# Optimization experiments

Hardware: AMD Instinct MI355X
Metric: run time of the kernel (lower is better)

## Reference

```python
import jax, jax.numpy as jnp
import numpy as np

COMPRESSION = 2  # max-pool factor along flattened spatial axis for phi and g


def setup_inputs() -> dict:
    key = jax.random.key(0)
    ks = jax.random.split(key, 5)
    B, C, H, W = 4, 64, 96, 96
    Ci = 32  # intermediate_dim = C // 2
    s = 1.0 / np.sqrt(C)
    return {
        "x": jax.random.normal(ks[0], (B, C, H, W), dtype=jnp.float32),
        "w_theta": jax.random.normal(ks[1], (Ci, C), dtype=jnp.float32) * s,
        "b_theta": jnp.zeros((Ci,), dtype=jnp.float32),
        "w_phi": jax.random.normal(ks[2], (Ci, C), dtype=jnp.float32) * s,
        "b_phi": jnp.zeros((Ci,), dtype=jnp.float32),
        "w_g": jax.random.normal(ks[3], (Ci, C), dtype=jnp.float32) * s,
        "b_g": jnp.zeros((Ci,), dtype=jnp.float32),
        "w_out": jax.random.normal(ks[4], (C, Ci), dtype=jnp.float32) * (1.0 / np.sqrt(Ci)),
        "b_out": jnp.zeros((C,), dtype=jnp.float32),
    }


def reference(x, w_theta, b_theta, w_phi, b_phi, w_g, b_g, w_out, b_out):
    B, C, H, W = x.shape
    N = H * W
    xf = x.reshape(B, C, N).transpose(0, 2, 1)            # [B, N, C]
    # 1x1 conv projections == channel matmuls
    theta = xf @ w_theta.T + b_theta                      # [B, N, Ci]
    phi = xf @ w_phi.T + b_phi                            # [B, N, Ci]
    g = xf @ w_g.T + b_g                                  # [B, N, Ci]
    # compression: max-pool (kernel=stride=COMPRESSION) along flattened spatial axis
    Ci = theta.shape[-1]
    phi = phi.reshape(B, N // COMPRESSION, COMPRESSION, Ci).max(axis=2)  # [B, N/c, Ci]
    g = g.reshape(B, N // COMPRESSION, COMPRESSION, Ci).max(axis=2)      # [B, N/c, Ci]
    # embedded-gaussian affinity + softmax
    attn = jax.nn.softmax(jnp.einsum('bnc,bmc->bnm', theta, phi), axis=-1)  # [B, N, N/c]
    y = jnp.einsum('bnm,bmc->bnc', attn, g)               # [B, N, Ci]
    out = y @ w_out.T + b_out                             # [B, N, C]
    out = out.transpose(0, 2, 1).reshape(B, C, H, W)
    return out + x  # residual
```

## Files before the change

### kernel.cpp

```cpp
#include <hip/hip_runtime.h>
#include <hip/hip_bf16.h>


#define NQ 9216
#define MM 4608
#define TPW 36
#define LOG2E 1.44269504088896340736f

typedef __attribute__((ext_vector_type(8))) short bf16x8;
typedef __attribute__((ext_vector_type(4))) float f32x4;
typedef __attribute__((ext_vector_type(4))) unsigned short u16x4;

static __device__ __forceinline__ unsigned pk2(float a, float b) {
    __hip_bfloat162 h = __float22bfloat162_rn(make_float2(a, b));
    return *reinterpret_cast<unsigned*>(&h);
}

__global__ __launch_bounds__(128, 4) void proj_kernel(
    const float* __restrict__ x,
    const float* __restrict__ wt, const float* __restrict__ bt,
    const float* __restrict__ wp, const float* __restrict__ bp,
    const float* __restrict__ wg, const float* __restrict__ bg,
    unsigned short* __restrict__ theta, unsigned short* __restrict__ phi,
    unsigned short* __restrict__ gT)
{
    __shared__ unsigned short gst[32 * 20];

    const int tid  = threadIdx.x;
    const int wid  = tid >> 6;
    const int lane = tid & 63;
    const int q = lane >> 4;
    const int c = lane & 15;

    const int b     = blockIdx.x / 288;
    const int rem   = blockIdx.x % 288;
    const int n0    = rem * 32 + wid * 16;

    const float* Wm[3] = {wt, wp, wg};
    const float* Bm[3] = {bt, bp, bg};

    bf16x8 wf[3][2][2];
    float bias[3][2];
#pragma unroll
    for (int p = 0; p < 3; ++p) {
#pragma unroll
        for (int ct = 0; ct < 2; ++ct) {
            bias[p][ct] = Bm[p][ct * 16 + c];
#pragma unroll
            for (int ks = 0; ks < 2; ++ks) {
                const float* wsrc = Wm[p] + (ct * 16 + c) * 64 + ks * 32 + q * 8;
                f32x4 w0 = *(const f32x4*)wsrc;
                f32x4 w1 = *(const f32x4*)(wsrc + 4);
                unsigned* wk = (unsigned*)&wf[p][ct][ks];
                wk[0] = pk2(w0[0], w0[1]); wk[1] = pk2(w0[2], w0[3]);
                wk[2] = pk2(w1[0], w1[1]); wk[3] = pk2(w1[2], w1[3]);
            }
        }
    }

    bf16x8 af[2];
#pragma unroll
    for (int ks = 0; ks < 2; ++ks) {
        unsigned* ap = (unsigned*)&af[ks];
#pragma unroll
        for (int j2 = 0; j2 < 4; ++j2) {
            float x0 = x[(b * 64 + ks * 32 + q * 8 + j2 * 2) * NQ + n0 + c];
            float x1 = x[(b * 64 + ks * 32 + q * 8 + j2 * 2 + 1) * NQ + n0 + c];
            ap[j2] = pk2(x0, x1);
        }
    }

#pragma unroll
    for (int p = 0; p < 3; ++p) {
#pragma unroll
        for (int ct = 0; ct < 2; ++ct) {
            f32x4 acc = {0.f, 0.f, 0.f, 0.f};
            acc = __builtin_amdgcn_mfma_f32_16x16x32_bf16(af[0], wf[p][ct][0], acc, 0, 0, 0);
            acc = __builtin_amdgcn_mfma_f32_16x16x32_bf16(af[1], wf[p][ct][1], acc, 0, 0, 0);
#pragma unroll
            for (int r = 0; r < 4; ++r) acc[r] += bias[p][ct];
            const int ci = ct * 16 + c;
            if (p == 0) {
                unsigned pv0 = pk2(acc[0] * LOG2E, acc[1] * LOG2E);
                unsigned pv1 = pk2(acc[2] * LOG2E, acc[3] * LOG2E);
                theta[(b * NQ + n0 + 4 * q + 0) * 32 + ci] = (unsigned short)pv0;
                theta[(b * NQ + n0 + 4 * q + 1) * 32 + ci] = (unsigned short)(pv0 >> 16);
                theta[(b * NQ + n0 + 4 * q + 2) * 32 + ci] = (unsigned short)pv1;
                theta[(b * NQ + n0 + 4 * q + 3) * 32 + ci] = (unsigned short)(pv1 >> 16);
            } else {
                unsigned pv = pk2(fmaxf(acc[0], acc[1]), fmaxf(acc[2], acc[3]));
                if (p == 1) {
                    const int m0 = (n0 >> 1) + 2 * q;
                    phi[(b * MM + m0) * 32 + ci]     = (unsigned short)pv;
                    phi[(b * MM + m0 + 1) * 32 + ci] = (unsigned short)(pv >> 16);
                } else {
                    *(unsigned int*)(gst + ci * 20 + wid * 8 + 2 * q) = pv;
                }
            }
        }
    }

    __syncthreads();
    {
        const int ci = tid >> 2;
        const int m4 = (tid & 3) * 4;
        u16x4 v = *(const u16x4*)(gst + ci * 20 + m4);
        *(u16x4*)(gT + (b * 32 + ci) * MM + rem * 16 + m4) = v;
    }
}

__global__ __launch_bounds__(256, 4) void attn_kernel(
    const unsigned short* __restrict__ theta, const unsigned short* __restrict__ phi,
    const unsigned short* __restrict__ gT,
    unsigned short* __restrict__ y)
{
    __shared__ unsigned short pld[4][48 * 32];
    __shared__ float red[4][48][36];
    __shared__ float lred[4][48];

    const int tid  = threadIdx.x;
    const int w    = tid >> 6;
    const int lane = tid & 63;
    const int q  = lane >> 4;
    const int c  = lane & 15;
    const int sw = ((c >> 1) & 3) << 3;

    const int b  = blockIdx.x / 192;
    const int nb = (blockIdx.x % 192) * 48;

    bf16x8 qf[3];
#pragma unroll
    for (int rt = 0; rt < 3; ++rt)
        qf[rt] = *(const bf16x8*)(theta + (b * NQ + nb + rt * 16 + c) * 32 + q * 8);

    const unsigned short* phiB = phi + (size_t)b * MM * 32;
    const unsigned short* gTB  = gT + (size_t)b * 32 * MM;
    unsigned short* myp = pld[w];

    f32x4 acc[3][2];
    float lsum[3];
#pragma unroll
    for (int rt = 0; rt < 3; ++rt) {
        lsum[rt] = 0.f;
#pragma unroll
        for (int s2 = 0; s2 < 2; ++s2) acc[rt][s2] = (f32x4){0.f, 0.f, 0.f, 0.f};
    }

    const int t0 = w * TPW;
    bf16x8 kf[2], vf[2];

#define LOAD_KF(m0) do {                                                      \
    kf[0] = *(const bf16x8*)(phiB + ((m0) + c) * 32 + q * 8);                 \
    kf[1] = *(const bf16x8*)(phiB + ((m0) + 16 + c) * 32 + q * 8);            \
} while (0)

#define LOAD_VF(m0) do {                                                      \
    vf[0] = *(const bf16x8*)(gTB + c * MM + (m0) + q * 8);                    \
    vf[1] = *(const bf16x8*)(gTB + (16 + c) * MM + (m0) + q * 8);             \
} while (0)

#define S_STEP(rt) do {                                                      \
    _Pragma("unroll")                                                        \
    for (int mct = 0; mct < 2; ++mct) {                                      \
        f32x4 z = {0.f, 0.f, 0.f, 0.f};                                      \
        f32x4 s = __builtin_amdgcn_mfma_f32_16x16x32_bf16(kf[mct], qf[rt], z, 0, 0, 0); \
        float e0 = __builtin_amdgcn_exp2f(s[0]);                             \
        float e1 = __builtin_amdgcn_exp2f(s[1]);                             \
        float e2 = __builtin_amdgcn_exp2f(s[2]);                             \
        float e3 = __builtin_amdgcn_exp2f(s[3]);                             \
        lsum[rt] += (e0 + e1) + (e2 + e3);                                   \
        uint2 hv = {pk2(e0, e1), pk2(e2, e3)};                               \
        *(uint2*)(myp + (((rt) * 16 + c) << 5) + ((mct * 16 + 4 * q) ^ sw)) = hv; \
    }                                                                        \
} while (0)

#define PV_STEP(rt) do {                                                     \
    bf16x8 pf = *(const bf16x8*)(myp + (((rt) * 16 + c) << 5) + ((q * 8) ^ sw)); \
    acc[rt][0] = __builtin_amdgcn_mfma_f32_16x16x32_bf16(vf[0], pf, acc[rt][0], 0, 0, 0); \
    acc[rt][1] = __builtin_amdgcn_mfma_f32_16x16x32_bf16(vf[1], pf, acc[rt][1], 0, 0, 0); \
} while (0)

    LOAD_KF(t0 * 32);
    LOAD_VF(t0 * 32);
    S_STEP(0); S_STEP(1); S_STEP(2);

    for (int mi = 1; mi < TPW; ++mi) {
        const int m0 = (t0 + mi) * 32;
        LOAD_KF(m0);
        PV_STEP(0); PV_STEP(1); PV_STEP(2);
        LOAD_VF(m0);
        S_STEP(0); S_STEP(1); S_STEP(2);
    }

    PV_STEP(0); PV_STEP(1); PV_STEP(2);

#undef LOAD_KF
#undef LOAD_VF
#undef S_STEP
#undef PV_STEP

#pragma unroll
    for (int rt = 0; rt < 3; ++rt) {
        float v = lsum[rt];
        v += __shfl_xor(v, 16);
        v += __shfl_xor(v, 32);
        if (lane < 16) lred[w][rt * 16 + lane] = v;
    }
#pragma unroll
    for (int rt = 0; rt < 3; ++rt)
#pragma unroll
        for (int s2 = 0; s2 < 2; ++s2)
            *(f32x4*)&red[w][rt * 16 + c][s2 * 16 + 4 * q] = acc[rt][s2];

    __syncthreads();

    {
        const int n   = tid & 63;
        const int cig = (tid >> 6) * 8;
        if (n < 48) {
            float ls = (lred[0][n] + lred[1][n]) + (lred[2][n] + lred[3][n]);
            float inv = 1.0f / ls;
            f32x4 s0 = {0.f, 0.f, 0.f, 0.f}, s1 = {0.f, 0.f, 0.f, 0.f};
#pragma unroll
            for (int ww = 0; ww < 4; ++ww) {
                s0 += *(const f32x4*)&red[ww][n][cig];
                s1 += *(const f32x4*)&red[ww][n][cig + 4];
            }
            unsigned short* yb = y + (size_t)(b * 32 + cig) * NQ + nb + n;
#pragma unroll
            for (int k = 0; k < 4; ++k) {
                yb[(size_t)k * NQ]       = (unsigned short)(pk2(s0[k] * inv, 0.f) & 0xffff);
                yb[(size_t)(k + 4) * NQ] = (unsigned short)(pk2(s1[k] * inv, 0.f) & 0xffff);
            }
        }
    }
}

__global__ __launch_bounds__(128, 4) void oproj_kernel(
    const unsigned short* __restrict__ y,
    const float* __restrict__ w_out, const float* __restrict__ b_out,
    const float* __restrict__ x, float* __restrict__ out)
{
    __shared__ unsigned short yld[32 * 36];

    const int tid = threadIdx.x;
    const int b   = blockIdx.x / 288;
    const int nb  = (blockIdx.x % 288) * 32;

    {
        const int ci = tid >> 2;
        const int n8 = (tid & 3) * 8;
        const unsigned short* yr = y + (size_t)(b * 32 + ci) * NQ + nb + n8;
        uint2 v0 = *(const uint2*)yr;
        uint2 v1 = *(const uint2*)(yr + 4);
        *(uint2*)(yld + ci * 36 + n8)     = v0;
        *(uint2*)(yld + ci * 36 + n8 + 4) = v1;
    }
    __syncthreads();

    const int w    = tid >> 6;
    const int lane = tid & 63;
    const int q = lane >> 4;
    const int c = lane & 15;

    bf16x8 wof[4];
#pragma unroll
    for (int ct = 0; ct < 4; ++ct) {
        const float* wsrc = w_out + (ct * 16 + c) * 32 + q * 8;
        f32x4 w0 = *(const f32x4*)wsrc;
        f32x4 w1 = *(const f32x4*)(wsrc + 4);
        unsigned* wk = (unsigned*)&wof[ct];
        wk[0] = pk2(w0[0], w0[1]); wk[1] = pk2(w0[2], w0[3]);
        wk[2] = pk2(w1[0], w1[1]); wk[3] = pk2(w1[2], w1[3]);
    }

    bf16x8 yf;
    {
        unsigned short* yp = (unsigned short*)&yf;
#pragma unroll
        for (int j = 0; j < 8; ++j)
            yp[j] = yld[(q * 8 + j) * 36 + w * 16 + c];
    }

#pragma unroll
    for (int ct = 0; ct < 4; ++ct) {
        f32x4 z = {0.f, 0.f, 0.f, 0.f};
        f32x4 o = __builtin_amdgcn_mfma_f32_16x16x32_bf16(wof[ct], yf, z, 0, 0, 0);
#pragma unroll
        for (int r = 0; r < 4; ++r) {
            const int chn = ct * 16 + 4 * q + r;
            const size_t addr = (size_t)(b * 64 + chn) * NQ + nb + w * 16 + c;
            out[addr] = o[r] + b_out[chn] + x[addr];
        }
    }
}

extern "C" void kernel_launch(void* const* d_in, const int* in_sizes, int n_in,
                              void* d_out, int out_size, void* d_ws, size_t ws_size,
                              hipStream_t stream) {
    const float* x       = (const float*)d_in[0];
    const float* w_theta = (const float*)d_in[1];
    const float* b_theta = (const float*)d_in[2];
    const float* w_phi   = (const float*)d_in[3];
    const float* b_phi   = (const float*)d_in[4];
    const float* w_g     = (const float*)d_in[5];
    const float* b_g     = (const float*)d_in[6];
    const float* w_out   = (const float*)d_in[7];
    const float* b_out   = (const float*)d_in[8];
    float* out = (float*)d_out;

    unsigned short* theta = (unsigned short*)d_ws;
    unsigned short* phi   = theta + 4 * NQ * 32;
    unsigned short* gT    = phi + 4 * MM * 32;
    unsigned short* y     = gT + 4 * 32 * MM;

    proj_kernel<<<1152, 128, 0, stream>>>(x, w_theta, b_theta, w_phi, b_phi,
                                          w_g, b_g, theta, phi, gT);
    attn_kernel<<<768, 256, 0, stream>>>(theta, phi, gT, y);
    oproj_kernel<<<1152, 128, 0, stream>>>(y, w_out, b_out, x, out);
}
```

Before: 132.3 us.

## Fuse output projection into attention kernel and split key range over eight waves

The output 1x1 projection, bias and residual add move into the attention kernel's epilogue, so the separate oproj kernel and the bf16 y round trip through global memory go away. Each block now runs 8 waves, each covering half as many key tiles, and the two halves of the partial accumulators are combined in shared memory. Shared memory is unioned between the P staging buffers and the epilogue buffers to keep the footprint down. The cost is an extra reduction pass and more barriers in the epilogue, higher register pressure from the launch bounds of 512 threads with min 6 blocks, and only half the waves doing the projection MFMAs.

```diff
diff --git a/kernel.cpp b/kernel.cpp
--- a/kernel.cpp
+++ b/kernel.cpp
@@ -4,7 +4,7 @@
 
 #define NQ 9216
 #define MM 4608
-#define TPW 36
+#define TPW 18
 #define LOG2E 1.44269504088896340736f
 
 typedef __attribute__((ext_vector_type(8))) short bf16x8;
@@ -109,14 +109,20 @@
     }
 }
 
-__global__ __launch_bounds__(256, 4) void attn_kernel(
+__global__ __launch_bounds__(512, 6) void attn_kernel(
     const unsigned short* __restrict__ theta, const unsigned short* __restrict__ phi,
     const unsigned short* __restrict__ gT,
-    unsigned short* __restrict__ y)
+    const float* __restrict__ w_out, const float* __restrict__ b_out,
+    const float* __restrict__ x, float* __restrict__ out)
 {
-    __shared__ unsigned short pld[4][48 * 32];
-    __shared__ float red[4][48][36];
-    __shared__ float lred[4][48];
+    __shared__ union SharedU {
+        unsigned short pld[8][48 * 32];
+        struct {
+            float red[4][48][36];
+            float lred[4][48];
+            unsigned short yld[32][50];
+        } ep;
+    } sh;
 
     const int tid  = threadIdx.x;
     const int w    = tid >> 6;
@@ -135,7 +141,7 @@
 
     const unsigned short* phiB = phi + (size_t)b * MM * 32;
     const unsigned short* gTB  = gT + (size_t)b * 32 * MM;
-    unsigned short* myp = pld[w];
+    unsigned short* myp = sh.pld[w];
 
     f32x4 acc[3][2];
     float lsum[3];
@@ -199,98 +205,90 @@
 #undef S_STEP
 #undef PV_STEP
 
+    float lv[3];
 #pragma unroll
     for (int rt = 0; rt < 3; ++rt) {
         float v = lsum[rt];
         v += __shfl_xor(v, 16);
         v += __shfl_xor(v, 32);
-        if (lane < 16) lred[w][rt * 16 + lane] = v;
-    }
-#pragma unroll
-    for (int rt = 0; rt < 3; ++rt)
-#pragma unroll
-        for (int s2 = 0; s2 < 2; ++s2)
-            *(f32x4*)&red[w][rt * 16 + c][s2 * 16 + 4 * q] = acc[rt][s2];
-
-    __syncthreads();
-
-    {
-        const int n   = tid & 63;
-        const int cig = (tid >> 6) * 8;
-        if (n < 48) {
-            float ls = (lred[0][n] + lred[1][n]) + (lred[2][n] + lred[3][n]);
-            float inv = 1.0f / ls;
-            f32x4 s0 = {0.f, 0.f, 0.f, 0.f}, s1 = {0.f, 0.f, 0.f, 0.f};
-#pragma unroll
-            for (int ww = 0; ww < 4; ++ww) {
-                s0 += *(const f32x4*)&red[ww][n][cig];
-                s1 += *(const f32x4*)&red[ww][n][cig + 4];
+        lv[rt] = v;
+    }
+
+    __syncthreads();
+
+    if (w < 4) {
+        if (lane < 16) {
+            sh.ep.lred[w][lane]      = lv[0];
+            sh.ep.lred[w][16 + lane] = lv[1];
+            sh.ep.lred[w][32 + lane] = lv[2];
+        }
+#pragma unroll
+        for (int rt = 0; rt < 3; ++rt)
+#pragma unroll
+            for (int s2 = 0; s2 < 2; ++s2)
+                *(f32x4*)&sh.ep.red[w][rt * 16 + c][s2 * 16 + 4 * q] = acc[rt][s2];
+    }
+    __syncthreads();
+
+    if (w >= 4) {
+        const int tw = w - 4;
+        if (lane < 16) {
+            sh.ep.lred[tw][lane]      += lv[0];
+            sh.ep.lred[tw][16 + lane] += lv[1];
+            sh.ep.lred[tw][32 + lane] += lv[2];
+        }
+#pragma unroll
+        for (int rt = 0; rt < 3; ++rt)
+#pragma unroll
+            for (int s2 = 0; s2 < 2; ++s2) {
+                float* p = &sh.ep.red[tw][rt * 16 + c][s2 * 16 + 4 * q];
+                f32x4 cur = *(f32x4*)p;
+                *(f32x4*)p = cur + acc[rt][s2];
             }
-            unsigned short* yb = y + (size_t)(b * 32 + cig) * NQ + nb + n;
-#pragma unroll
-            for (int k = 0; k < 4; ++k) {
-                yb[(size_t)k * NQ]       = (unsigned short)(pk2(s0[k] * inv, 0.f) & 0xffff);
-                yb[(size_t)(k + 4) * NQ] = (unsigned short)(pk2(s1[k] * inv, 0.f) & 0xffff);
+    }
+    __syncthreads();
+
+    if (tid < 384) {
+        const int n  = tid % 48;
+        const int cg = (tid / 48) * 4;
+        float ls = (sh.ep.lred[0][n] + sh.ep.lred[1][n]) +
+                   (sh.ep.lred[2][n] + sh.ep.lred[3][n]);
+        float inv = 1.0f / ls;
+        f32x4 s = {0.f, 0.f, 0.f, 0.f};
+#pragma unroll
+        for (int ww = 0; ww < 4; ++ww)
+            s += *(const f32x4*)&sh.ep.red[ww][n][cg];
+#pragma unroll
+        for (int k = 0; k < 4; ++k)
+            sh.ep.yld[cg + k][n] = (unsigned short)(pk2(s[k] * inv, 0.f) & 0xffff);
+    }
+    __syncthreads();
+
+    if (w < 4) {
+        bf16x8 wof;
+        {
+            const float* wsrc = w_out + (w * 16 + c) * 32 + q * 8;
+            f32x4 w0 = *(const f32x4*)wsrc;
+            f32x4 w1 = *(const f32x4*)(wsrc + 4);
+            unsigned* wk = (unsigned*)&wof;
+            wk[0] = pk2(w0[0], w0[1]); wk[1] = pk2(w0[2], w0[3]);
+            wk[2] = pk2(w1[0], w1[1]); wk[3] = pk2(w1[2], w1[3]);
+        }
+#pragma unroll
+        for (int nt = 0; nt < 3; ++nt) {
+            bf16x8 yf;
+            unsigned short* yp = (unsigned short*)&yf;
+#pragma unroll
+            for (int j = 0; j < 8; ++j)
+                yp[j] = sh.ep.yld[q * 8 + j][nt * 16 + c];
+            f32x4 z = {0.f, 0.f, 0.f, 0.f};
+            f32x4 o = __builtin_amdgcn_mfma_f32_16x16x32_bf16(wof, yf, z, 0, 0, 0);
+#pragma unroll
+            for (int r = 0; r < 4; ++r) {
+                const int chn = w * 16 + 4 * q + r;
+                const size_t addr = (size_t)(b * 64 + chn) * NQ + nb + nt * 16 + c;
+                out[addr] = o[r] + b_out[chn] + x[addr];
             }
-        }
-    }
-}
-
-__global__ __launch_bounds__(128, 4) void oproj_kernel(
-    const unsigned short* __restrict__ y,
-    const float* __restrict__ w_out, const float* __restrict__ b_out,
-    const float* __restrict__ x, float* __restrict__ out)
-{
-    __shared__ unsigned short yld[32 * 36];
-
-    const int tid = threadIdx.x;
-    const int b   = blockIdx.x / 288;
-    const int nb  = (blockIdx.x % 288) * 32;
-
-    {
-        const int ci = tid >> 2;
-        const int n8 = (tid & 3) * 8;
-        const unsigned short* yr = y + (size_t)(b * 32 + ci) * NQ + nb + n8;
-        uint2 v0 = *(const uint2*)yr;
-        uint2 v1 = *(const uint2*)(yr + 4);
-        *(uint2*)(yld + ci * 36 + n8)     = v0;
-        *(uint2*)(yld + ci * 36 + n8 + 4) = v1;
-    }
-    __syncthreads();
-
-    const int w    = tid >> 6;
-    const int lane = tid & 63;
-    const int q = lane >> 4;
-    const int c = lane & 15;
-
-    bf16x8 wof[4];
-#pragma unroll
-    for (int ct = 0; ct < 4; ++ct) {
-        const float* wsrc = w_out + (ct * 16 + c) * 32 + q * 8;
-        f32x4 w0 = *(const f32x4*)wsrc;
-        f32x4 w1 = *(const f32x4*)(wsrc + 4);
-        unsigned* wk = (unsigned*)&wof[ct];
-        wk[0] = pk2(w0[0], w0[1]); wk[1] = pk2(w0[2], w0[3]);
-        wk[2] = pk2(w1[0], w1[1]); wk[3] = pk2(w1[2], w1[3]);
-    }
-
-    bf16x8 yf;
-    {
-        unsigned short* yp = (unsigned short*)&yf;
-#pragma unroll
-        for (int j = 0; j < 8; ++j)
-            yp[j] = yld[(q * 8 + j) * 36 + w * 16 + c];
-    }
-
-#pragma unroll
-    for (int ct = 0; ct < 4; ++ct) {
-        f32x4 z = {0.f, 0.f, 0.f, 0.f};
-        f32x4 o = __builtin_amdgcn_mfma_f32_16x16x32_bf16(wof[ct], yf, z, 0, 0, 0);
-#pragma unroll
-        for (int r = 0; r < 4; ++r) {
-            const int chn = ct * 16 + 4 * q + r;
-            const size_t addr = (size_t)(b * 64 + chn) * NQ + nb + w * 16 + c;
-            out[addr] = o[r] + b_out[chn] + x[addr];
         }
     }
 }
@@ -312,10 +310,8 @@
     unsigned short* theta = (unsigned short*)d_ws;
     unsigned short* phi   = theta + 4 * NQ * 32;
     unsigned short* gT    = phi + 4 * MM * 32;
-    unsigned short* y     = gT + 4 * 32 * MM;
 
     proj_kernel<<<1152, 128, 0, stream>>>(x, w_theta, b_theta, w_phi, b_phi,
                                           w_g, b_g, theta, phi, gT);
-    attn_kernel<<<768, 256, 0, stream>>>(theta, phi, gT, y);
-    oproj_kernel<<<1152, 128, 0, stream>>>(y, w_out, b_out, x, out);
+    attn_kernel<<<768, 512, 0, stream>>>(theta, phi, gT, w_out, b_out, x, out);
 }
```

Result: slower. 146.5 us (+10.7%).
